# Kernel optimization log

Hardware: AMD Instinct MI355X
Metric: run time of the kernel (lower is better)

Reference implementation:

```python
import jax, jax.numpy as jnp
import numpy as np

P = 64
K = 64
D = 2048
KERNEL_MUL = 2.0
KERNEL_NUM = 5


def setup_inputs() -> dict:
    key = jax.random.key(0)
    k1, k2 = jax.random.split(key)
    source = jax.random.normal(k1, (P * K, D), dtype=jnp.float32)
    target = jax.random.normal(k2, (P * K, D), dtype=jnp.float32)
    return {"source": source, "target": target}


def _mmd_terms(source, target):
    # split into P groups of K rows each, process all splits at once
    src = source.reshape(P, K, D)
    tgt = target.reshape(P, K, D)
    total = jnp.concatenate([src, tgt], axis=1)          # [P, 2K, D]
    n = 2 * K
    # pairwise squared L2 distances per split: [P, 2K, 2K]
    sq = jnp.sum(total * total, axis=-1)                  # [P, 2K]
    gram = jnp.einsum('pid,pjd->pij', total, total)       # [P, 2K, 2K]
    l2 = sq[:, :, None] + sq[:, None, :] - 2.0 * gram
    # bandwidth from detached distances (torch uses L2_distance.data)
    bw = jax.lax.stop_gradient(jnp.sum(l2, axis=(1, 2))) / (n * n - n)  # [P]
    bw = bw / (KERNEL_MUL ** (KERNEL_NUM // 2))
    mults = KERNEL_MUL ** jnp.arange(KERNEL_NUM, dtype=jnp.float32)     # [kn]
    bws = bw[:, None] * mults[None, :] + 1e-9                           # [P, kn]
    # multi-bandwidth Gaussian kernel sum: [P, 2K, 2K]
    kern = jnp.sum(jnp.exp(-l2[:, None, :, :] / bws[:, :, None, None]), axis=1)
    XX = kern[:, :K, :K]
    YY = kern[:, K:, K:]
    XY = kern[:, :K, K:]
    YX = kern[:, K:, :K]
    xx = jnp.mean(XX, axis=(1, 2))
    yy = jnp.mean(YY, axis=(1, 2))
    xy = jnp.mean(XY, axis=(1, 2))
    yx = jnp.mean(YX, axis=(1, 2))
    per_split_loss = xx + yy - xy - yx                    # [P]
    total_loss = jnp.sum(per_split_loss) / P
    return total_loss, l2, xx, yy, xy, yx


def reference(source, target):
    total_loss, l2, xx, yy, xy, yx = _mmd_terms(source, target)
    # original returns max of l2dist from the LAST split only
    max_l2_last = jnp.max(l2[-1])
    return (total_loss.reshape(1), max_l2_last,
            jnp.sum(xx) / P, jnp.sum(yy) / P, jnp.sum(xy) / P, jnp.sum(yx) / P)
```

## Files before the change

### kernel.cpp

```cpp
#include <hip/hip_runtime.h>

typedef _Float16 half8 __attribute__((ext_vector_type(8)));
typedef float floatx4 __attribute__((ext_vector_type(4)));
typedef unsigned int uint2v __attribute__((ext_vector_type(2)));

#define NSPLIT 64
#define KS 64
#define DIM 2048
#define NROW 128
#define BK 128
#define KSPL 4
#define KCH (DIM / KSPL)
#define NKC_A (KCH / BK)
#define SST 152
#define GSZ (NROW * NROW)

__device__ __forceinline__ unsigned int pk16(float a, float b) {
  return __builtin_bit_cast(unsigned int, __builtin_amdgcn_cvt_pkrtz(a, b));
}

__global__ void init_out_kernel(float* out) {
  if (threadIdx.x < 6) out[threadIdx.x] = 0.0f;
}

__global__ __launch_bounds__(1024) void gram_kernel(const float* __restrict__ src,
                                                    const float* __restrict__ tgt,
                                                    float* __restrict__ ws) {
  __shared__ __align__(16) _Float16 stage[NROW * SST];

  const int p = blockIdx.x >> 2;
  const int c = blockIdx.x & (KSPL - 1);
  const int tid = threadIdx.x;
  const int lane = tid & 63;
  const int wave = tid >> 6;

  const int srow = tid >> 3;
  const int c4 = (tid & 7) * 4;
  const float* rowp = ((srow < KS) ? (src + (size_t)(p * KS + srow) * DIM)
                                   : (tgt + (size_t)(p * KS + (srow - KS)) * DIM)) +
                      c * KCH;

  const int wr = (wave >> 2) * 32;
  const int wc = (wave & 3) * 32;
  const int fr = lane & 15;
  const int fk = (lane >> 4) * 8;

  floatx4 acc00 = {0.f, 0.f, 0.f, 0.f};
  floatx4 acc01 = {0.f, 0.f, 0.f, 0.f};
  floatx4 acc10 = {0.f, 0.f, 0.f, 0.f};
  floatx4 acc11 = {0.f, 0.f, 0.f, 0.f};

  float4 f0, f1, f2, f3;
#define LOADK(kc)                                      \
  do {                                                 \
    const float* gp_ = rowp + (kc) * BK + c4;          \
    f0 = *(const float4*)(gp_);                        \
    f1 = *(const float4*)(gp_ + 32);                   \
    f2 = *(const float4*)(gp_ + 64);                   \
    f3 = *(const float4*)(gp_ + 96);                   \
  } while (0)

  LOADK(0);
  for (int kc = 0; kc < NKC_A; ++kc) {
    __syncthreads();
    {
      _Float16* sp = &stage[srow * SST + c4];
      *(uint2v*)(sp)      = (uint2v){pk16(f0.x, f0.y), pk16(f0.z, f0.w)};
      *(uint2v*)(sp + 32) = (uint2v){pk16(f1.x, f1.y), pk16(f1.z, f1.w)};
      *(uint2v*)(sp + 64) = (uint2v){pk16(f2.x, f2.y), pk16(f2.z, f2.w)};
      *(uint2v*)(sp + 96) = (uint2v){pk16(f3.x, f3.y), pk16(f3.z, f3.w)};
    }
    __syncthreads();
    if (kc + 1 < NKC_A) LOADK(kc + 1);
#pragma unroll
    for (int ks = 0; ks < 4; ++ks) {
      const int ko = ks * 32 + fk;
      half8 a0 = *(const half8*)&stage[(wr + fr) * SST + ko];
      half8 a1 = *(const half8*)&stage[(wr + 16 + fr) * SST + ko];
      half8 b0 = *(const half8*)&stage[(wc + fr) * SST + ko];
      half8 b1 = *(const half8*)&stage[(wc + 16 + fr) * SST + ko];
      acc00 = __builtin_amdgcn_mfma_f32_16x16x32_f16(a0, b0, acc00, 0, 0, 0);
      acc01 = __builtin_amdgcn_mfma_f32_16x16x32_f16(a0, b1, acc01, 0, 0, 0);
      acc10 = __builtin_amdgcn_mfma_f32_16x16x32_f16(a1, b0, acc10, 0, 0, 0);
      acc11 = __builtin_amdgcn_mfma_f32_16x16x32_f16(a1, b1, acc11, 0, 0, 0);
    }
  }
#undef LOADK

  float* wsp = ws + (size_t)blockIdx.x * GSZ;
  const int ccol = lane & 15;
  const int crow = (lane >> 4) * 4;
#pragma unroll
  for (int r = 0; r < 4; ++r) {
    wsp[(wr + crow + r) * NROW + (wc + ccol)] = acc00[r];
    wsp[(wr + crow + r) * NROW + (wc + 16 + ccol)] = acc01[r];
    wsp[(wr + 16 + crow + r) * NROW + (wc + ccol)] = acc10[r];
    wsp[(wr + 16 + crow + r) * NROW + (wc + 16 + ccol)] = acc11[r];
  }
}

__global__ __launch_bounds__(1024) void reduce_kernel(const float* __restrict__ ws,
                                                      float* __restrict__ out) {
  __shared__ float sqv[NROW];
  __shared__ float reds[16];
  __shared__ float redm[16];
  __shared__ float quad[4];
  __shared__ float bcast[8];

  const int p = blockIdx.x;
  const int tid = threadIdx.x;
  const int lane = tid & 63;
  const int wave = tid >> 6;

  const int row = tid >> 3;
  const int c0 = (tid & 7) * 16;

  const float* base = ws + (size_t)p * KSPL * GSZ + row * NROW + c0;
  float4 g0 = {0.f, 0.f, 0.f, 0.f}, g1 = g0, g2 = g0, g3 = g0;
#pragma unroll
  for (int c = 0; c < KSPL; ++c) {
    const float* bp = base + (size_t)c * GSZ;
    float4 t0 = *(const float4*)(bp);
    float4 t1 = *(const float4*)(bp + 4);
    float4 t2 = *(const float4*)(bp + 8);
    float4 t3 = *(const float4*)(bp + 12);
    g0.x += t0.x; g0.y += t0.y; g0.z += t0.z; g0.w += t0.w;
    g1.x += t1.x; g1.y += t1.y; g1.z += t1.z; g1.w += t1.w;
    g2.x += t2.x; g2.y += t2.y; g2.z += t2.z; g2.w += t2.w;
    g3.x += t3.x; g3.y += t3.y; g3.z += t3.z; g3.w += t3.w;
  }
  float gs[16] = {g0.x, g0.y, g0.z, g0.w, g1.x, g1.y, g1.z, g1.w,
                  g2.x, g2.y, g2.z, g2.w, g3.x, g3.y, g3.z, g3.w};

  if ((tid & 7) == (row >> 4)) sqv[row] = gs[row & 15];
  if (tid < 4) quad[tid] = 0.0f;
  __syncthreads();

  float l2r[16];
  float lsum = 0.0f;
  float lmax = -1e30f;
  const float sqi = sqv[row];
#pragma unroll
  for (int m = 0; m < 16; ++m) {
    float v = sqi + sqv[c0 + m] - 2.0f * gs[m];
    l2r[m] = v;
    lsum += v;
    lmax = fmaxf(lmax, v);
  }
#pragma unroll
  for (int m = 1; m <= 32; m <<= 1) {
    lsum += __shfl_xor(lsum, m, 64);
    lmax = fmaxf(lmax, __shfl_xor(lmax, m, 64));
  }
  if (lane == 0) {
    reds[wave] = lsum;
    redm[wave] = lmax;
  }
  __syncthreads();
  if (tid == 0) {
    float tot = 0.0f, mx = -1e30f;
    for (int w = 0; w < 16; ++w) {
      tot += reds[w];
      mx = fmaxf(mx, redm[w]);
    }
    float bw = tot / (float)(NROW * NROW - NROW) * 0.25f;
    float mult = 1.0f;
    for (int k = 0; k < 5; ++k) {
      bcast[k] = 1.0f / (bw * mult + 1e-9f);
      mult *= 2.0f;
    }
    if (p == NSPLIT - 1) out[1] = mx;
  }
  __syncthreads();

  const float ib0 = bcast[0], ib1 = bcast[1], ib2 = bcast[2], ib3 = bcast[3], ib4 = bcast[4];
  float qsum = 0.0f;
#pragma unroll
  for (int m = 0; m < 16; ++m) {
    float v = l2r[m];
    qsum += __expf(-v * ib0) + __expf(-v * ib1) + __expf(-v * ib2) +
            __expf(-v * ib3) + __expf(-v * ib4);
  }
  qsum += __shfl_xor(qsum, 1, 64);
  qsum += __shfl_xor(qsum, 2, 64);
  qsum += __shfl_xor(qsum, 8, 64);
  qsum += __shfl_xor(qsum, 16, 64);
  qsum += __shfl_xor(qsum, 32, 64);
  if (lane == 0 || lane == 4) {
    int q = (wave >= 8 ? 2 : 0) + ((lane >> 2) & 1);
    atomicAdd(&quad[q], qsum);
  }
  __syncthreads();

  if (tid == 0) {
    const float inv = 1.0f / (4096.0f * 64.0f);
    float xx = quad[0], xy = quad[1], yx = quad[2], yy = quad[3];
    atomicAdd(&out[0], (xx + yy - xy - yx) * inv);
    atomicAdd(&out[2], xx * inv);
    atomicAdd(&out[3], yy * inv);
    atomicAdd(&out[4], xy * inv);
    atomicAdd(&out[5], yx * inv);
  }
}

extern "C" void kernel_launch(void* const* d_in, const int* in_sizes, int n_in,
                              void* d_out, int out_size, void* d_ws, size_t ws_size,
                              hipStream_t stream) {
  const float* src = (const float*)d_in[0];
  const float* tgt = (const float*)d_in[1];
  float* out = (float*)d_out;
  float* ws = (float*)d_ws;
  init_out_kernel<<<1, 64, 0, stream>>>(out);
  gram_kernel<<<NSPLIT * KSPL, 1024, 0, stream>>>(src, tgt, ws);
  reduce_kernel<<<NSPLIT, 1024, 0, stream>>>(ws, out);
}
```

Measured before the change: 112.8 us.

## Split gram K-dimension finer and split reduce rows across four blocks per split

The gram kernel now splits the feature dimension into 8 chunks instead of 4, doubling the grid. Each gram block also atomically accumulates its total Gram sum per split. That sum lets the bandwidth be computed analytically as 2N*sum(sq) - 2*sum(G) instead of through a full block reduction. The reduce kernel is then split into four row-blocks per split, with the diagonal read directly and the last-split max combined via an integer atomicMax. This raises parallelism in both kernels, at the cost of twice the workspace traffic for partial Grams plus extra atomics.

```diff
diff --git a/kernel.cpp b/kernel.cpp
--- a/kernel.cpp
+++ b/kernel.cpp
@@ -9,26 +9,29 @@
 #define DIM 2048
 #define NROW 128
 #define BK 128
-#define KSPL 4
+#define KSPL 8
 #define KCH (DIM / KSPL)
 #define NKC_A (KCH / BK)
 #define SST 152
 #define GSZ (NROW * NROW)
+#define GT_OFF (NSPLIT * KSPL * GSZ)
 
 __device__ __forceinline__ unsigned int pk16(float a, float b) {
   return __builtin_bit_cast(unsigned int, __builtin_amdgcn_cvt_pkrtz(a, b));
 }
 
-__global__ void init_out_kernel(float* out) {
+__global__ void init_kernel(float* out, float* ws) {
   if (threadIdx.x < 6) out[threadIdx.x] = 0.0f;
+  if (threadIdx.x < NSPLIT) ws[GT_OFF + threadIdx.x] = 0.0f;
 }
 
 __global__ __launch_bounds__(1024) void gram_kernel(const float* __restrict__ src,
                                                     const float* __restrict__ tgt,
                                                     float* __restrict__ ws) {
   __shared__ __align__(16) _Float16 stage[NROW * SST];
-
-  const int p = blockIdx.x >> 2;
+  __shared__ float red[16];
+
+  const int p = blockIdx.x >> 3;
   const int c = blockIdx.x & (KSPL - 1);
   const int tid = threadIdx.x;
   const int lane = tid & 63;
@@ -90,116 +93,126 @@
   float* wsp = ws + (size_t)blockIdx.x * GSZ;
   const int ccol = lane & 15;
   const int crow = (lane >> 4) * 4;
+  float gsum = 0.0f;
 #pragma unroll
   for (int r = 0; r < 4; ++r) {
     wsp[(wr + crow + r) * NROW + (wc + ccol)] = acc00[r];
     wsp[(wr + crow + r) * NROW + (wc + 16 + ccol)] = acc01[r];
     wsp[(wr + 16 + crow + r) * NROW + (wc + ccol)] = acc10[r];
     wsp[(wr + 16 + crow + r) * NROW + (wc + 16 + ccol)] = acc11[r];
+    gsum += acc00[r] + acc01[r] + acc10[r] + acc11[r];
+  }
+#pragma unroll
+  for (int m = 1; m <= 32; m <<= 1) gsum += __shfl_xor(gsum, m, 64);
+  if (lane == 0) red[wave] = gsum;
+  __syncthreads();
+  if (tid == 0) {
+    float t = 0.0f;
+    for (int w = 0; w < 16; ++w) t += red[w];
+    atomicAdd(&ws[GT_OFF + p], t);
   }
 }
 
 __global__ __launch_bounds__(1024) void reduce_kernel(const float* __restrict__ ws,
                                                       float* __restrict__ out) {
   __shared__ float sqv[NROW];
-  __shared__ float reds[16];
+  __shared__ float bcast[8];
   __shared__ float redm[16];
-  __shared__ float quad[4];
-  __shared__ float bcast[8];
-
-  const int p = blockIdx.x;
+  __shared__ float quad2[2];
+
+  const int p = blockIdx.x >> 2;
+  const int rb = blockIdx.x & 3;
   const int tid = threadIdx.x;
   const int lane = tid & 63;
   const int wave = tid >> 6;
 
-  const int row = tid >> 3;
-  const int c0 = (tid & 7) * 16;
-
-  const float* base = ws + (size_t)p * KSPL * GSZ + row * NROW + c0;
-  float4 g0 = {0.f, 0.f, 0.f, 0.f}, g1 = g0, g2 = g0, g3 = g0;
-#pragma unroll
-  for (int c = 0; c < KSPL; ++c) {
-    const float* bp = base + (size_t)c * GSZ;
-    float4 t0 = *(const float4*)(bp);
-    float4 t1 = *(const float4*)(bp + 4);
-    float4 t2 = *(const float4*)(bp + 8);
-    float4 t3 = *(const float4*)(bp + 12);
-    g0.x += t0.x; g0.y += t0.y; g0.z += t0.z; g0.w += t0.w;
-    g1.x += t1.x; g1.y += t1.y; g1.z += t1.z; g1.w += t1.w;
-    g2.x += t2.x; g2.y += t2.y; g2.z += t2.z; g2.w += t2.w;
-    g3.x += t3.x; g3.y += t3.y; g3.z += t3.z; g3.w += t3.w;
-  }
-  float gs[16] = {g0.x, g0.y, g0.z, g0.w, g1.x, g1.y, g1.z, g1.w,
-                  g2.x, g2.y, g2.z, g2.w, g3.x, g3.y, g3.z, g3.w};
-
-  if ((tid & 7) == (row >> 4)) sqv[row] = gs[row & 15];
-  if (tid < 4) quad[tid] = 0.0f;
-  __syncthreads();
-
-  float l2r[16];
-  float lsum = 0.0f;
-  float lmax = -1e30f;
-  const float sqi = sqv[row];
-#pragma unroll
-  for (int m = 0; m < 16; ++m) {
-    float v = sqi + sqv[c0 + m] - 2.0f * gs[m];
-    l2r[m] = v;
-    lsum += v;
-    lmax = fmaxf(lmax, v);
-  }
-#pragma unroll
-  for (int m = 1; m <= 32; m <<= 1) {
-    lsum += __shfl_xor(lsum, m, 64);
-    lmax = fmaxf(lmax, __shfl_xor(lmax, m, 64));
-  }
-  if (lane == 0) {
-    reds[wave] = lsum;
-    redm[wave] = lmax;
-  }
-  __syncthreads();
+  const int lr = tid >> 5;
+  const int cg = tid & 31;
+  const int row = rb * 32 + lr;
+
+  const float* base = ws + (size_t)(p * KSPL) * GSZ + row * NROW + cg * 4;
+  float4 g = {0.f, 0.f, 0.f, 0.f};
+#pragma unroll
+  for (int c8 = 0; c8 < KSPL; ++c8) {
+    float4 t = *(const float4*)(base + (size_t)c8 * GSZ);
+    g.x += t.x; g.y += t.y; g.z += t.z; g.w += t.w;
+  }
+
+  if (tid < NROW) {
+    const float* dp = ws + (size_t)(p * KSPL) * GSZ + tid * (NROW + 1);
+    float d = 0.0f;
+#pragma unroll
+    for (int c8 = 0; c8 < KSPL; ++c8) d += dp[(size_t)c8 * GSZ];
+    sqv[tid] = d;
+  }
+  if (tid < 2) quad2[tid] = 0.0f;
+  __syncthreads();
+
   if (tid == 0) {
-    float tot = 0.0f, mx = -1e30f;
-    for (int w = 0; w < 16; ++w) {
-      tot += reds[w];
-      mx = fmaxf(mx, redm[w]);
-    }
-    float bw = tot / (float)(NROW * NROW - NROW) * 0.25f;
+    float ssq = 0.0f;
+    for (int i = 0; i < NROW; ++i) ssq += sqv[i];
+    float gt = ws[GT_OFF + p];
+    float suml2 = 2.0f * (float)NROW * ssq - 2.0f * gt;
+    float bw = suml2 / (float)(NROW * NROW - NROW) * 0.25f;
     float mult = 1.0f;
     for (int k = 0; k < 5; ++k) {
       bcast[k] = 1.0f / (bw * mult + 1e-9f);
       mult *= 2.0f;
     }
-    if (p == NSPLIT - 1) out[1] = mx;
-  }
-  __syncthreads();
+  }
+  __syncthreads();
+
+  const float sqi = sqv[row];
+  float l2r[4];
+  float lmax = 0.0f;
+#pragma unroll
+  for (int k = 0; k < 4; ++k) {
+    float v = sqi + sqv[cg * 4 + k] - 2.0f * ((const float*)&g)[k];
+    l2r[k] = v;
+    lmax = fmaxf(lmax, v);
+  }
+
+  if (p == NSPLIT - 1) {
+#pragma unroll
+    for (int m = 1; m <= 32; m <<= 1) lmax = fmaxf(lmax, __shfl_xor(lmax, m, 64));
+    if (lane == 0) redm[wave] = lmax;
+    __syncthreads();
+    if (tid == 0) {
+      float mx = 0.0f;
+      for (int w = 0; w < 16; ++w) mx = fmaxf(mx, redm[w]);
+      atomicMax((int*)(out + 1), __float_as_int(mx));
+    }
+  }
 
   const float ib0 = bcast[0], ib1 = bcast[1], ib2 = bcast[2], ib3 = bcast[3], ib4 = bcast[4];
   float qsum = 0.0f;
 #pragma unroll
-  for (int m = 0; m < 16; ++m) {
-    float v = l2r[m];
+  for (int k = 0; k < 4; ++k) {
+    float v = l2r[k];
     qsum += __expf(-v * ib0) + __expf(-v * ib1) + __expf(-v * ib2) +
             __expf(-v * ib3) + __expf(-v * ib4);
   }
   qsum += __shfl_xor(qsum, 1, 64);
   qsum += __shfl_xor(qsum, 2, 64);
+  qsum += __shfl_xor(qsum, 4, 64);
   qsum += __shfl_xor(qsum, 8, 64);
-  qsum += __shfl_xor(qsum, 16, 64);
   qsum += __shfl_xor(qsum, 32, 64);
-  if (lane == 0 || lane == 4) {
-    int q = (wave >= 8 ? 2 : 0) + ((lane >> 2) & 1);
-    atomicAdd(&quad[q], qsum);
-  }
+  if (lane == 0) atomicAdd(&quad2[0], qsum);
+  if (lane == 16) atomicAdd(&quad2[1], qsum);
   __syncthreads();
 
   if (tid == 0) {
     const float inv = 1.0f / (4096.0f * 64.0f);
-    float xx = quad[0], xy = quad[1], yx = quad[2], yy = quad[3];
-    atomicAdd(&out[0], (xx + yy - xy - yx) * inv);
-    atomicAdd(&out[2], xx * inv);
-    atomicAdd(&out[3], yy * inv);
-    atomicAdd(&out[4], xy * inv);
-    atomicAdd(&out[5], yx * inv);
+    float qx = quad2[0], qy = quad2[1];
+    if (rb < 2) {
+      atomicAdd(&out[0], (qx - qy) * inv);
+      atomicAdd(&out[2], qx * inv);
+      atomicAdd(&out[4], qy * inv);
+    } else {
+      atomicAdd(&out[0], (qy - qx) * inv);
+      atomicAdd(&out[3], qy * inv);
+      atomicAdd(&out[5], qx * inv);
+    }
   }
 }
 
@@ -210,7 +223,7 @@
   const float* tgt = (const float*)d_in[1];
   float* out = (float*)d_out;
   float* ws = (float*)d_ws;
-  init_out_kernel<<<1, 64, 0, stream>>>(out);
+  init_kernel<<<1, 64, 0, stream>>>(out, ws);
   gram_kernel<<<NSPLIT * KSPL, 1024, 0, stream>>>(src, tgt, ws);
-  reduce_kernel<<<NSPLIT, 1024, 0, stream>>>(ws, out);
-}
+  reduce_kernel<<<NSPLIT * 4, 1024, 0, stream>>>(ws, out);
+}
```

Measured after the change: 123.0 us. 1.09x slower.
